# Kernel tuning notes

Hardware: AMD Instinct MI355X
Metric: run time of the kernel (lower is better)

Reference implementation:

```python
import jax, jax.numpy as jnp
import numpy as np

ALPHA = 0.1
THETA = 0.5
LAYERS = 4
N, E, D_IN, H, D_OUT = 100000, 1600000, 128, 128, 128


def setup_inputs() -> dict:
    key = jax.random.key(0)
    ks = jax.random.split(key, 9)
    x = jax.random.normal(ks[0], (N, D_IN), jnp.float32)
    edge_src = jax.random.randint(ks[1], (E,), 0, N, jnp.int32)
    edge_dst = jax.random.randint(ks[2], (E,), 0, N, jnp.int32)
    edge_w = jax.random.uniform(ks[3], (E,), jnp.float32)
    s_in = 1.0 / np.sqrt(D_IN)
    s_h = 1.0 / np.sqrt(H)
    W0 = jax.random.uniform(ks[4], (D_IN, H), jnp.float32, -s_in, s_in)
    b0 = jax.random.uniform(ks[5], (H,), jnp.float32, -s_in, s_in)
    W1 = jax.random.uniform(ks[6], (H, D_OUT), jnp.float32, -s_h, s_h)
    b1 = jax.random.uniform(ks[7], (D_OUT,), jnp.float32, -s_h, s_h)
    glorot = np.sqrt(6.0 / (H + H))
    convW = jax.random.uniform(ks[8], (LAYERS, H, H), jnp.float32, -glorot, glorot)
    return dict(x=x, edge_src=edge_src, edge_dst=edge_dst, edge_w=edge_w,
                W0=W0, b0=b0, W1=W1, b1=b1, convW=convW)


def reference(x, edge_src, edge_dst, edge_w, W0, b0, W1, b1, convW):
    # input projection + relu; x_0 is the initial residual (GCNII)
    h = jax.nn.relu(x @ W0 + b0)
    x0 = h
    for l in range(LAYERS):
        beta = float(np.log(THETA / (l + 1) + 1.0))
        # SpMM: agg[i] = sum_{(j->i) in E} w_e * h[j]
        msg = h[edge_src] * edge_w[:, None]                      # [E, H]
        agg = jax.ops.segment_sum(msg, edge_dst, num_segments=N)  # [N, H]
        out = (1.0 - ALPHA) * agg + ALPHA * x0                    # initial residual
        out = (1.0 - beta) * out + beta * (out @ convW[l])        # identity mapping
        h = jax.nn.relu(out)
    logits = h @ W1 + b1
    return jax.nn.log_softmax(logits, axis=-1)
```

## Files before the change

kernel.cpp:

```cpp
#include <hip/hip_runtime.h>
#include <math.h>

typedef unsigned int uint;
typedef unsigned short ushort;
typedef unsigned char uchar;
using bf8   = __attribute__((ext_vector_type(8))) short;
using f32x4 = __attribute__((ext_vector_type(4))) float;
using f32x2 = __attribute__((ext_vector_type(2))) float;

__device__ inline ushort f2bf(float f) {
  uint u = __float_as_uint(f);
  return (ushort)((u + 0x7fffu + ((u >> 16) & 1u)) >> 16);
}
__device__ inline float bf2f(ushort s) { return __uint_as_float(((uint)s) << 16); }
__device__ inline uint packbf2(float a, float b) {
  uint ua = __float_as_uint(a), ub = __float_as_uint(b);
  ua = (ua + 0x7fffu + ((ua >> 16) & 1u)) >> 16;
  ub = (ub + 0x7fffu + ((ub >> 16) & 1u)) & 0xffff0000u;
  return ua | ub;
}
__device__ inline float bflo(uint u) { return __uint_as_float(u << 16); }
__device__ inline float bfhi(uint u) { return __uint_as_float(u & 0xffff0000u); }

#if __has_builtin(__builtin_amdgcn_cvt_pk_f32_fp8)
template<bool W>
__device__ inline f32x2 fp8x2_f32(uint v) {
  return __builtin_amdgcn_cvt_pk_f32_fp8((int)v, W);
}
#else
__device__ inline float fp8_1(uint b) {
  uint e = (b >> 3) & 15u, m = b & 7u;
  float nrm = __uint_as_float(((e + 120u) << 23) | (m << 20));
  float sub = (float)m * 0.001953125f;
  return e ? nrm : sub;
}
template<bool W>
__device__ inline f32x2 fp8x2_f32(uint v) {
  uint sh = W ? 16u : 0u;
  f32x2 r; r.x = fp8_1((v >> sh) & 0xffu); r.y = fp8_1((v >> (sh + 8)) & 0xffu);
  return r;
}
#endif

__device__ inline uint f32_fp8(float f) {
  if (!(f > 0.f)) return 0u;
  if (f >= 446.f) return 0x7eu;
  if (f < 0.015625f) return (uint)(f * 512.f + 0.5f);
  uint u = __float_as_uint(f);
  uint r = u + 0x7ffffu + ((u >> 20) & 1u);
  uint eb = r >> 23, mant = (r >> 20) & 7u;
  if (eb > 135u || (eb == 135u && mant == 7u)) return 0x7eu;
  return ((eb - 120u) << 3) | mant;
}

__global__ void hist_k(const int* __restrict__ dst, int* __restrict__ cnt, int E) {
  int tid = blockIdx.x * blockDim.x + threadIdx.x;
  int stride4 = gridDim.x * blockDim.x * 4;
  for (int base = tid * 4; base + 3 < E; base += stride4) {
    int4 d = *(const int4*)&dst[base];
    atomicAdd(&cnt[d.x], 1);
    atomicAdd(&cnt[d.y], 1);
    atomicAdd(&cnt[d.z], 1);
    atomicAdd(&cnt[d.w], 1);
  }
  int tail0 = (E & ~3);
  int e = tail0 + tid;
  if (e < E) atomicAdd(&cnt[dst[e]], 1);
}

__global__ __launch_bounds__(256) void scanA_k(const int* __restrict__ cnt,
                                               int* __restrict__ bsum, int N) {
  __shared__ int red[256];
  int tid = threadIdx.x;
  int i0 = blockIdx.x * 1024 + tid * 4;
  int s = 0;
  #pragma unroll
  for (int k = 0; k < 4; ++k) { int i = i0 + k; if (i < N) s += cnt[i]; }
  red[tid] = s;
  __syncthreads();
  for (int off = 128; off; off >>= 1) {
    if (tid < off) red[tid] += red[tid + off];
    __syncthreads();
  }
  if (tid == 0) bsum[blockIdx.x] = red[0];
}

__global__ __launch_bounds__(128) void scanB_k(const int* __restrict__ bsum,
                                               int* __restrict__ bbase, int nb) {
  __shared__ int buf[2][128];
  int tid = threadIdx.x;
  buf[0][tid] = (tid < nb) ? bsum[tid] : 0;
  __syncthreads();
  int pin = 0;
  for (int off = 1; off < 128; off <<= 1) {
    int x = buf[pin][tid];
    if (tid >= off) x += buf[pin][tid - off];
    buf[1 - pin][tid] = x;
    __syncthreads();
    pin = 1 - pin;
  }
  if (tid < nb) bbase[tid] = (tid == 0) ? 0 : buf[pin][tid - 1];
}

__global__ __launch_bounds__(256) void scanC_k(const int* __restrict__ cnt,
    const int* __restrict__ bbase, int* __restrict__ rp, int N, int E) {
  __shared__ int buf[2][256];
  int tid = threadIdx.x;
  int i0 = blockIdx.x * 1024 + tid * 4;
  int c[4]; int s = 0;
  #pragma unroll
  for (int k = 0; k < 4; ++k) { int i = i0 + k; c[k] = (i < N) ? cnt[i] : 0; s += c[k]; }
  buf[0][tid] = s;
  __syncthreads();
  int pin = 0;
  for (int off = 1; off < 256; off <<= 1) {
    int x = buf[pin][tid];
    if (tid >= off) x += buf[pin][tid - off];
    buf[1 - pin][tid] = x;
    __syncthreads();
    pin = 1 - pin;
  }
  int run = bbase[blockIdx.x] + buf[pin][tid] - s;
  #pragma unroll
  for (int k = 0; k < 4; ++k) {
    int i = i0 + k;
    if (i < N) { rp[i] = run; run += c[k]; }
  }
  if (blockIdx.x == 0 && tid == 0) rp[N] = E;
}

__global__ __launch_bounds__(256) void scatter_k(const int* __restrict__ src,
    const int* __restrict__ dst, const float* __restrict__ w,
    const int* __restrict__ rp, int* __restrict__ cnt,
    uint* __restrict__ epk, int E, int N) {
  int part = blockIdx.x & 7;
  int slice = blockIdx.x >> 3;
  int nslices = gridDim.x >> 3;
  int E4 = E >> 2;
  int per4 = (E4 + nslices - 1) / nslices;
  int lo4 = slice * per4, hi4 = min(E4, lo4 + per4);
  int nper = (N + 7) >> 3;
  int nlo = part * nper, nhi = min(N, nlo + nper);
#define PUT(D, EIDX) do { \
    int d_ = (D); \
    if (d_ >= nlo && d_ < nhi) { \
      int off_ = atomicAdd(&cnt[d_], -1) - 1; \
      uint wq_ = (uint)(w[EIDX] * 32767.f + 0.5f); \
      epk[rp[d_] + off_] = ((uint)src[EIDX] << 15) | wq_; \
    } \
  } while (0)
  for (int q = lo4 + threadIdx.x; q < hi4; q += 256) {
    int4 d4 = ((const int4*)dst)[q];
    int e = q << 2;
    PUT(d4.x, e);
    PUT(d4.y, e + 1);
    PUT(d4.z, e + 2);
    PUT(d4.w, e + 3);
  }
  if (slice == 0) {
    for (int e = (E & ~3) + threadIdx.x; e < E; e += 256) PUT(dst[e], e);
  }
#undef PUT
}

__global__ __launch_bounds__(256) void prepW_k(const float* __restrict__ W0,
    const float* __restrict__ convW, const float* __restrict__ W1,
    ushort* __restrict__ Wt) {
  int b = blockIdx.x;
  int m = b >> 4;
  int n0 = (b & 15) * 8;
  const float* W = (m == 0) ? W0 : (m <= 4) ? (convW + (size_t)(m - 1) * 128 * 128) : W1;
  ushort* dst = Wt + (size_t)m * 128 * 128;
  int t = threadIdx.x;
  int n = n0 + (t >> 5);
  int k0 = (t & 31) * 4;
  float a = W[(size_t)(k0 + 0) * 128 + n];
  float c = W[(size_t)(k0 + 1) * 128 + n];
  float d = W[(size_t)(k0 + 2) * 128 + n];
  float e = W[(size_t)(k0 + 3) * 128 + n];
  *(uint2*)&dst[(size_t)n * 128 + k0] = make_uint2(packbf2(a, c), packbf2(d, e));
}

__global__ __launch_bounds__(256) void spmm_k(const int* __restrict__ rp,
    const uint* __restrict__ epk, const uchar* __restrict__ h8,
    const ushort* __restrict__ x0bf, ushort* __restrict__ outbf, int N) {
  int node = (blockIdx.x * blockDim.x + threadIdx.x) >> 4;
  int l16 = threadIdx.x & 15;
  if (node >= N) return;
  int b = rp[node], e = rp[node + 1];
  float a0 = 0.f, a1 = 0.f, a2 = 0.f, a3 = 0.f;
  float a4 = 0.f, a5 = 0.f, a6 = 0.f, a7 = 0.f;
  const uint2* hb = (const uint2*)h8;
#define EDG(EU, HV) do { \
    float wgt = (float)((EU) & 0x7fffu) * (1.f / 32767.f); \
    f32x2 p0 = fp8x2_f32<false>((HV).x), p1 = fp8x2_f32<true>((HV).x); \
    f32x2 p2 = fp8x2_f32<false>((HV).y), p3 = fp8x2_f32<true>((HV).y); \
    a0 = fmaf(wgt, p0.x, a0); a1 = fmaf(wgt, p0.y, a1); \
    a2 = fmaf(wgt, p1.x, a2); a3 = fmaf(wgt, p1.y, a3); \
    a4 = fmaf(wgt, p2.x, a4); a5 = fmaf(wgt, p2.y, a5); \
    a6 = fmaf(wgt, p3.x, a6); a7 = fmaf(wgt, p3.y, a7); \
  } while (0)
  int j = b;
  for (; j + 7 < e; j += 8) {
    uint u0 = epk[j],     u1 = epk[j + 1], u2 = epk[j + 2], u3 = epk[j + 3];
    uint u4 = epk[j + 4], u5 = epk[j + 5], u6 = epk[j + 6], u7 = epk[j + 7];
    uint2 h0 = hb[(size_t)(u0 >> 15) * 16 + l16];
    uint2 h1 = hb[(size_t)(u1 >> 15) * 16 + l16];
    uint2 h2 = hb[(size_t)(u2 >> 15) * 16 + l16];
    uint2 h3 = hb[(size_t)(u3 >> 15) * 16 + l16];
    uint2 h4 = hb[(size_t)(u4 >> 15) * 16 + l16];
    uint2 h5 = hb[(size_t)(u5 >> 15) * 16 + l16];
    uint2 h6 = hb[(size_t)(u6 >> 15) * 16 + l16];
    uint2 h7 = hb[(size_t)(u7 >> 15) * 16 + l16];
    EDG(u0, h0); EDG(u1, h1); EDG(u2, h2); EDG(u3, h3);
    EDG(u4, h4); EDG(u5, h5); EDG(u6, h6); EDG(u7, h7);
  }
  for (; j + 3 < e; j += 4) {
    uint u0 = epk[j], u1 = epk[j + 1], u2 = epk[j + 2], u3 = epk[j + 3];
    uint2 h0 = hb[(size_t)(u0 >> 15) * 16 + l16];
    uint2 h1 = hb[(size_t)(u1 >> 15) * 16 + l16];
    uint2 h2 = hb[(size_t)(u2 >> 15) * 16 + l16];
    uint2 h3 = hb[(size_t)(u3 >> 15) * 16 + l16];
    EDG(u0, h0); EDG(u1, h1); EDG(u2, h2); EDG(u3, h3);
  }
  for (; j < e; ++j) {
    uint u0 = epk[j];
    uint2 h0 = hb[(size_t)(u0 >> 15) * 16 + l16];
    EDG(u0, h0);
  }
#undef EDG
  uint4 xv = ((const uint4*)x0bf)[(size_t)node * 16 + l16];
  float o0 = 0.9f * a0 + 0.1f * bflo(xv.x);
  float o1 = 0.9f * a1 + 0.1f * bfhi(xv.x);
  float o2 = 0.9f * a2 + 0.1f * bflo(xv.y);
  float o3 = 0.9f * a3 + 0.1f * bfhi(xv.y);
  float o4 = 0.9f * a4 + 0.1f * bflo(xv.z);
  float o5 = 0.9f * a5 + 0.1f * bfhi(xv.z);
  float o6 = 0.9f * a6 + 0.1f * bflo(xv.w);
  float o7 = 0.9f * a7 + 0.1f * bfhi(xv.w);
  uint4 u;
  u.x = packbf2(o0, o1); u.y = packbf2(o2, o3);
  u.z = packbf2(o4, o5); u.w = packbf2(o6, o7);
  ((uint4*)outbf)[(size_t)node * 16 + l16] = u;
}

template<int MODE, int ABF, int OUT8>
__global__ __launch_bounds__(256, 4) void gemm_mfma(const void* __restrict__ inv,
    const ushort* __restrict__ Wt, const float* __restrict__ bias,
    float* __restrict__ outf, ushort* __restrict__ outbf, ushort* __restrict__ outbf2,
    uchar* __restrict__ out8, float cin, float cw, int N) {
  const float*  inf = (const float*)inv;
  const ushort* inb = (const ushort*)inv;
  int tid = threadIdx.x;
  int w = tid >> 6, lane = tid & 63;
  int l15 = lane & 15, hi = lane >> 4;
  int rbase = blockIdx.x * 128 + w * 32;

  f32x4 acc[2][8];
  #pragma unroll
  for (int mi = 0; mi < 2; ++mi)
    #pragma unroll
    for (int ni = 0; ni < 8; ++ni)
      acc[mi][ni] = (f32x4){0.f, 0.f, 0.f, 0.f};

  int r0 = min(rbase + l15, N - 1);
  int r1 = min(rbase + 16 + l15, N - 1);

  #pragma unroll
  for (int kt = 0; kt < 4; ++kt) {
    int koff = kt * 32 + hi * 8;
    bf8 a0, a1;
    if (ABF) {
      a0 = *(const bf8*)&inb[(size_t)r0 * 128 + koff];
      a1 = *(const bf8*)&inb[(size_t)r1 * 128 + koff];
    } else {
      float4 f0 = *(const float4*)&inf[(size_t)r0 * 128 + koff];
      float4 f1 = *(const float4*)&inf[(size_t)r0 * 128 + koff + 4];
      float4 g0 = *(const float4*)&inf[(size_t)r1 * 128 + koff];
      float4 g1 = *(const float4*)&inf[(size_t)r1 * 128 + koff + 4];
      union { bf8 v; uint u[4]; } ta, tb;
      ta.u[0] = packbf2(f0.x, f0.y); ta.u[1] = packbf2(f0.z, f0.w);
      ta.u[2] = packbf2(f1.x, f1.y); ta.u[3] = packbf2(f1.z, f1.w);
      tb.u[0] = packbf2(g0.x, g0.y); tb.u[1] = packbf2(g0.z, g0.w);
      tb.u[2] = packbf2(g1.x, g1.y); tb.u[3] = packbf2(g1.z, g1.w);
      a0 = ta.v; a1 = tb.v;
    }
    #pragma unroll
    for (int ni = 0; ni < 8; ++ni) {
      bf8 b = *(const bf8*)&Wt[(size_t)(ni * 16 + l15) * 128 + koff];
      acc[0][ni] = __builtin_amdgcn_mfma_f32_16x16x32_bf16(a0, b, acc[0][ni], 0, 0, 0);
      acc[1][ni] = __builtin_amdgcn_mfma_f32_16x16x32_bf16(a1, b, acc[1][ni], 0, 0, 0);
    }
  }

  float bcol[8];
  if (MODE != 1) {
    #pragma unroll
    for (int ni = 0; ni < 8; ++ni) bcol[ni] = bias[ni * 16 + l15];
  }

  #pragma unroll
  for (int mi = 0; mi < 2; ++mi) {
    #pragma unroll
    for (int reg = 0; reg < 4; ++reg) {
      int row = rbase + mi * 16 + 4 * hi + reg;
      bool valid = (row < N);
      float y[8];
      #pragma unroll
      for (int ni = 0; ni < 8; ++ni) y[ni] = acc[mi][ni][reg];
      if (MODE == 1) {
        if (valid) {
          #pragma unroll
          for (int ni = 0; ni < 8; ++ni) {
            float iv = bf2f(inb[(size_t)row * 128 + ni * 16 + l15]);
            y[ni] = fmaxf(cin * iv + cw * y[ni], 0.f);
          }
        }
      } else {
        #pragma unroll
        for (int ni = 0; ni < 8; ++ni) y[ni] += bcol[ni];
        if (MODE == 0) {
          #pragma unroll
          for (int ni = 0; ni < 8; ++ni) y[ni] = fmaxf(y[ni], 0.f);
        }
      }
      if (MODE == 2) {
        float m = y[0];
        #pragma unroll
        for (int ni = 1; ni < 8; ++ni) m = fmaxf(m, y[ni]);
        #pragma unroll
        for (int off = 1; off <= 8; off <<= 1) m = fmaxf(m, __shfl_xor(m, off));
        float s = 0.f;
        #pragma unroll
        for (int ni = 0; ni < 8; ++ni) s += expf(y[ni] - m);
        #pragma unroll
        for (int off = 1; off <= 8; off <<= 1) s += __shfl_xor(s, off);
        float lg = m + logf(s);
        #pragma unroll
        for (int ni = 0; ni < 8; ++ni) y[ni] -= lg;
      }
      if (valid) {
        if (MODE == 2) {
          #pragma unroll
          for (int ni = 0; ni < 8; ++ni)
            outf[(size_t)row * 128 + ni * 16 + l15] = y[ni];
        } else {
          #pragma unroll
          for (int ni = 0; ni < 8; ++ni) {
            size_t idx = (size_t)row * 128 + ni * 16 + l15;
            if (OUT8) out8[idx] = (uchar)f32_fp8(y[ni]);
            else      outbf[idx] = f2bf(y[ni]);
            if (MODE == 0) outbf2[idx] = f2bf(y[ni]);
          }
        }
      }
    }
  }
}

extern "C" void kernel_launch(void* const* d_in, const int* in_sizes, int n_in,
                              void* d_out, int out_size, void* d_ws, size_t ws_size,
                              hipStream_t stream) {
  const float* x     = (const float*)d_in[0];
  const int*   esrc  = (const int*)d_in[1];
  const int*   edst  = (const int*)d_in[2];
  const float* ew    = (const float*)d_in[3];
  const float* W0    = (const float*)d_in[4];
  const float* b0    = (const float*)d_in[5];
  const float* W1    = (const float*)d_in[6];
  const float* b1    = (const float*)d_in[7];
  const float* convW = (const float*)d_in[8];
  int N = in_sizes[0] / 128;
  int E = in_sizes[1];
  float* outp = (float*)d_out;

  char* ws = (char*)d_ws;
  size_t off = 0;
  auto alloc = [&](size_t bytes) {
    void* p = ws + off;
    off += (bytes + 255) & ~(size_t)255;
    return p;
  };
  uchar*  h8    = (uchar*)alloc((size_t)N * 128);
  ushort* x0bf  = (ushort*)alloc((size_t)N * 128 * 2);
  ushort* bufB  = (ushort*)alloc((size_t)N * 128 * 2);
  ushort* bufA  = (ushort*)alloc((size_t)N * 128 * 2);
  ushort* Wtg   = (ushort*)alloc((size_t)6 * 128 * 128 * 2);
  int*    rp    = (int*)alloc((size_t)(N + 1) * 4);
  int*    cnt   = (int*)alloc((size_t)N * 4);
  uint*   epk   = (uint*)alloc((size_t)E * 4);
  int nbScan = (N + 1023) / 1024;
  int*    bsum  = (int*)alloc((size_t)nbScan * 4);
  int*    bbase = (int*)alloc((size_t)nbScan * 4);

  (void)hipMemsetAsync(cnt, 0, (size_t)N * 4, stream);
  hist_k<<<2048, 256, 0, stream>>>(edst, cnt, E);
  prepW_k<<<96, 256, 0, stream>>>(W0, convW, W1, Wtg);
  scanA_k<<<nbScan, 256, 0, stream>>>(cnt, bsum, N);
  scanB_k<<<1, 128, 0, stream>>>(bsum, bbase, nbScan);
  scanC_k<<<nbScan, 256, 0, stream>>>(cnt, bbase, rp, N, E);
  scatter_k<<<2048, 256, 0, stream>>>(esrc, edst, ew, rp, cnt, epk, E, N);

  int gemmBlocks = (N + 127) / 128;
  int spmmBlocks = (N + 15) / 16;

  gemm_mfma<0, 0, 1><<<gemmBlocks, 256, 0, stream>>>(
      x, Wtg, b0, nullptr, nullptr, x0bf, h8, 0.f, 1.f, N);

  for (int l = 0; l < 4; ++l) {
    float beta = logf(0.5f / (float)(l + 1) + 1.f);
    spmm_k<<<spmmBlocks, 256, 0, stream>>>(rp, epk, h8, x0bf, bufB, N);
    if (l < 3) {
      gemm_mfma<1, 1, 1><<<gemmBlocks, 256, 0, stream>>>(
          bufB, Wtg + (size_t)(1 + l) * 128 * 128, nullptr,
          nullptr, nullptr, nullptr, h8, 1.f - beta, beta, N);
    } else {
      gemm_mfma<1, 1, 0><<<gemmBlocks, 256, 0, stream>>>(
          bufB, Wtg + (size_t)(1 + l) * 128 * 128, nullptr,
          nullptr, bufA, nullptr, nullptr, 1.f - beta, beta, N);
    }
  }

  gemm_mfma<2, 1, 0><<<gemmBlocks, 256, 0, stream>>>(
      bufA, Wtg + (size_t)5 * 128 * 128, b1, outp, nullptr, nullptr, nullptr, 0.f, 1.f, N);
}
```

Measured before the change: 496.0 us.

## Bucket CSR edges by source range within each destination row

Builds the CSR with eight sub-buckets per destination node, keyed by the source index's high bits, so each row's edges are grouped by source region. This is meant to improve cache locality of the gathered fp8 feature rows during SpMM. The cost is an eight-times larger count and row-pointer array, which makes the histogram, scan and scatter passes heavier, plus an extra src read in the histogram.

```diff
diff --git a/kernel.cpp b/kernel.cpp
--- a/kernel.cpp
+++ b/kernel.cpp
@@ -7,6 +7,9 @@
 using bf8   = __attribute__((ext_vector_type(8))) short;
 using f32x4 = __attribute__((ext_vector_type(4))) float;
 using f32x2 = __attribute__((ext_vector_type(2))) float;
+using i32x4 = __attribute__((ext_vector_type(4))) int;
+
+#define RSH 14
 
 __device__ inline ushort f2bf(float f) {
   uint u = __float_as_uint(f);
@@ -53,29 +56,29 @@
   return ((eb - 120u) << 3) | mant;
 }
 
-__global__ void hist_k(const int* __restrict__ dst, int* __restrict__ cnt, int E) {
+__global__ void hist_k(const int* __restrict__ src, const int* __restrict__ dst,
+                       int* __restrict__ cnt, int E) {
   int tid = blockIdx.x * blockDim.x + threadIdx.x;
   int stride4 = gridDim.x * blockDim.x * 4;
   for (int base = tid * 4; base + 3 < E; base += stride4) {
-    int4 d = *(const int4*)&dst[base];
-    atomicAdd(&cnt[d.x], 1);
-    atomicAdd(&cnt[d.y], 1);
-    atomicAdd(&cnt[d.z], 1);
-    atomicAdd(&cnt[d.w], 1);
-  }
-  int tail0 = (E & ~3);
-  int e = tail0 + tid;
-  if (e < E) atomicAdd(&cnt[dst[e]], 1);
+    i32x4 d = *(const i32x4*)&dst[base];
+    i32x4 s = *(const i32x4*)&src[base];
+    atomicAdd(&cnt[d.x * 8 + (s.x >> RSH)], 1);
+    atomicAdd(&cnt[d.y * 8 + (s.y >> RSH)], 1);
+    atomicAdd(&cnt[d.z * 8 + (s.z >> RSH)], 1);
+    atomicAdd(&cnt[d.w * 8 + (s.w >> RSH)], 1);
+  }
+  int e = (E & ~3) + tid;
+  if (e < E) atomicAdd(&cnt[dst[e] * 8 + (src[e] >> RSH)], 1);
 }
 
 __global__ __launch_bounds__(256) void scanA_k(const int* __restrict__ cnt,
-                                               int* __restrict__ bsum, int N) {
+                                               int* __restrict__ bsum, int M) {
   __shared__ int red[256];
   int tid = threadIdx.x;
-  int i0 = blockIdx.x * 1024 + tid * 4;
+  int base = blockIdx.x * 8192 + tid * 32;
   int s = 0;
-  #pragma unroll
-  for (int k = 0; k < 4; ++k) { int i = i0 + k; if (i < N) s += cnt[i]; }
+  for (int k = 0; k < 32; ++k) { int i = base + k; if (i < M) s += cnt[i]; }
   red[tid] = s;
   __syncthreads();
   for (int off = 128; off; off >>= 1) {
@@ -103,13 +106,12 @@
 }
 
 __global__ __launch_bounds__(256) void scanC_k(const int* __restrict__ cnt,
-    const int* __restrict__ bbase, int* __restrict__ rp, int N, int E) {
+    const int* __restrict__ bbase, int* __restrict__ rp, int M, int E) {
   __shared__ int buf[2][256];
   int tid = threadIdx.x;
-  int i0 = blockIdx.x * 1024 + tid * 4;
-  int c[4]; int s = 0;
-  #pragma unroll
-  for (int k = 0; k < 4; ++k) { int i = i0 + k; c[k] = (i < N) ? cnt[i] : 0; s += c[k]; }
+  int base = blockIdx.x * 8192 + tid * 32;
+  int s = 0;
+  for (int k = 0; k < 32; ++k) { int i = base + k; if (i < M) s += cnt[i]; }
   buf[0][tid] = s;
   __syncthreads();
   int pin = 0;
@@ -121,17 +123,16 @@
     pin = 1 - pin;
   }
   int run = bbase[blockIdx.x] + buf[pin][tid] - s;
-  #pragma unroll
-  for (int k = 0; k < 4; ++k) {
-    int i = i0 + k;
-    if (i < N) { rp[i] = run; run += c[k]; }
-  }
-  if (blockIdx.x == 0 && tid == 0) rp[N] = E;
+  for (int k = 0; k < 32; ++k) {
+    int i = base + k;
+    if (i < M) { rp[i] = run; run += cnt[i]; }
+  }
+  if (blockIdx.x == 0 && tid == 0) rp[M] = E;
 }
 
 __global__ __launch_bounds__(256) void scatter_k(const int* __restrict__ src,
     const int* __restrict__ dst, const float* __restrict__ w,
-    const int* __restrict__ rp, int* __restrict__ cnt,
+    const int* __restrict__ rp8, int* __restrict__ cnt8,
     uint* __restrict__ epk, int E, int N) {
   int part = blockIdx.x & 7;
   int slice = blockIdx.x >> 3;
@@ -144,18 +145,21 @@
 #define PUT(D, EIDX) do { \
     int d_ = (D); \
     if (d_ >= nlo && d_ < nhi) { \
-      int off_ = atomicAdd(&cnt[d_], -1) - 1; \
+      uint s_ = (uint)src[EIDX]; \
+      int idx_ = d_ * 8 + (int)(s_ >> RSH); \
+      int off_ = atomicAdd(&cnt8[idx_], -1) - 1; \
       uint wq_ = (uint)(w[EIDX] * 32767.f + 0.5f); \
-      epk[rp[d_] + off_] = ((uint)src[EIDX] << 15) | wq_; \
+      epk[rp8[idx_] + off_] = (s_ << 15) | wq_; \
     } \
   } while (0)
   for (int q = lo4 + threadIdx.x; q < hi4; q += 256) {
-    int4 d4 = ((const int4*)dst)[q];
+    i32x4 d4 = *(const i32x4*)dst + 0, dd = ((const i32x4*)dst)[q];
     int e = q << 2;
-    PUT(d4.x, e);
-    PUT(d4.y, e + 1);
-    PUT(d4.z, e + 2);
-    PUT(d4.w, e + 3);
+    PUT(dd.x, e);
+    PUT(dd.y, e + 1);
+    PUT(dd.z, e + 2);
+    PUT(dd.w, e + 3);
+    (void)d4;
   }
   if (slice == 0) {
     for (int e = (E & ~3) + threadIdx.x; e < E; e += 256) PUT(dst[e], e);
@@ -181,13 +185,13 @@
   *(uint2*)&dst[(size_t)n * 128 + k0] = make_uint2(packbf2(a, c), packbf2(d, e));
 }
 
-__global__ __launch_bounds__(256) void spmm_k(const int* __restrict__ rp,
+__global__ __launch_bounds__(256) void spmm_k(const int* __restrict__ rp8,
     const uint* __restrict__ epk, const uchar* __restrict__ h8,
     const ushort* __restrict__ x0bf, ushort* __restrict__ outbf, int N) {
   int node = (blockIdx.x * blockDim.x + threadIdx.x) >> 4;
   int l16 = threadIdx.x & 15;
   if (node >= N) return;
-  int b = rp[node], e = rp[node + 1];
+  int b = rp8[node * 8], e = rp8[node * 8 + 8];
   float a0 = 0.f, a1 = 0.f, a2 = 0.f, a3 = 0.f;
   float a4 = 0.f, a5 = 0.f, a6 = 0.f, a7 = 0.f;
   const uint2* hb = (const uint2*)h8;
@@ -381,25 +385,26 @@
     off += (bytes + 255) & ~(size_t)255;
     return p;
   };
+  int M = N * 8;
   uchar*  h8    = (uchar*)alloc((size_t)N * 128);
   ushort* x0bf  = (ushort*)alloc((size_t)N * 128 * 2);
   ushort* bufB  = (ushort*)alloc((size_t)N * 128 * 2);
   ushort* bufA  = (ushort*)alloc((size_t)N * 128 * 2);
   ushort* Wtg   = (ushort*)alloc((size_t)6 * 128 * 128 * 2);
-  int*    rp    = (int*)alloc((size_t)(N + 1) * 4);
-  int*    cnt   = (int*)alloc((size_t)N * 4);
+  int*    rp8   = (int*)alloc((size_t)(M + 1) * 4);
+  int*    cnt8  = (int*)alloc((size_t)M * 4);
   uint*   epk   = (uint*)alloc((size_t)E * 4);
-  int nbScan = (N + 1023) / 1024;
+  int nbScan = (M + 8191) / 8192;
   int*    bsum  = (int*)alloc((size_t)nbScan * 4);
   int*    bbase = (int*)alloc((size_t)nbScan * 4);
 
-  (void)hipMemsetAsync(cnt, 0, (size_t)N * 4, stream);
-  hist_k<<<2048, 256, 0, stream>>>(edst, cnt, E);
+  (void)hipMemsetAsync(cnt8, 0, (size_t)M * 4, stream);
+  hist_k<<<2048, 256, 0, stream>>>(esrc, edst, cnt8, E);
   prepW_k<<<96, 256, 0, stream>>>(W0, convW, W1, Wtg);
-  scanA_k<<<nbScan, 256, 0, stream>>>(cnt, bsum, N);
+  scanA_k<<<nbScan, 256, 0, stream>>>(cnt8, bsum, M);
   scanB_k<<<1, 128, 0, stream>>>(bsum, bbase, nbScan);
-  scanC_k<<<nbScan, 256, 0, stream>>>(cnt, bbase, rp, N, E);
-  scatter_k<<<2048, 256, 0, stream>>>(esrc, edst, ew, rp, cnt, epk, E, N);
+  scanC_k<<<nbScan, 256, 0, stream>>>(cnt8, bbase, rp8, M, E);
+  scatter_k<<<2048, 256, 0, stream>>>(esrc, edst, ew, rp8, cnt8, epk, E, N);
 
   int gemmBlocks = (N + 127) / 128;
   int spmmBlocks = (N + 15) / 16;
@@ -409,7 +414,7 @@
 
   for (int l = 0; l < 4; ++l) {
     float beta = logf(0.5f / (float)(l + 1) + 1.f);
-    spmm_k<<<spmmBlocks, 256, 0, stream>>>(rp, epk, h8, x0bf, bufB, N);
+    spmm_k<<<spmmBlocks, 256, 0, stream>>>(rp8, epk, h8, x0bf, bufB, N);
     if (l < 3) {
       gemm_mfma<1, 1, 1><<<gemmBlocks, 256, 0, stream>>>(
           bufB, Wtg + (size_t)(1 + l) * 128 * 128, nullptr,
```

Result: slower. 514.8 us (+3.8%).
